# Performance work log

Hardware: AMD Instinct MI355X
Metric: run time of the kernel (lower is better)

Reference implementation:

```python
import jax, jax.numpy as jnp
import numpy as np
from jax import lax

D_MODEL = 1024
D_STATE = 128
D_CONV = 4
EXPAND = 2
HEADDIM = 64
D_INNER = EXPAND * D_MODEL          # 2048
NHEADS = D_INNER // HEADDIM         # 32
D_IN_PROJ = 2 * D_INNER + 2 * D_STATE + NHEADS  # 4384 (z, xBC, dt)
CONV_CH = D_INNER + 2 * D_STATE     # 2304
CHUNK = 128
EPS = 1e-5
BATCH, SEQ = 2, 2048


def silu(x):
    return x * jax.nn.sigmoid(x)


def rmsnorm(x, w):
    return x * lax.rsqrt(jnp.mean(x * x, axis=-1, keepdims=True) + EPS) * w


def segsum(a):
    # a: (b,h,c,q) -> (b,h,c,q,q); [i,j] = sum_{j<k<=i} a_k, -inf above diag
    q = a.shape[-1]
    cs = jnp.cumsum(a, axis=-1)
    seg = cs[..., :, None] - cs[..., None, :]
    mask = jnp.tril(jnp.ones((q, q), dtype=bool))
    return jnp.where(mask, seg, -jnp.inf)


def ssd(xh, dt, A, B, C):
    # xh: (b,l,h,p), dt: (b,l,h), A: (h,), B,C: (b,l,n). Chunked SSD scan.
    b, l, h, p = xh.shape
    n = B.shape[-1]
    c = l // CHUNK
    X = (xh * dt[..., None]).reshape(b, c, CHUNK, h, p)
    Adt = (A * dt).reshape(b, c, CHUNK, h).transpose(0, 3, 1, 2)  # (b,h,c,q)
    Bc = B.reshape(b, c, CHUNK, n)
    Cc = C.reshape(b, c, CHUNK, n)
    Acs = jnp.cumsum(Adt, axis=-1)
    L = jnp.exp(segsum(Adt))  # (b,h,c,q,q) causal decay within chunk
    Y_diag = jnp.einsum('bcln,bcsn,bhcls,bcshp->bclhp', Cc, Bc, L, X)
    decay_states = jnp.exp(Acs[..., -1:] - Acs)
    states = jnp.einsum('bcln,bhcl,bclhp->bchpn', Bc, decay_states, X)
    chunk_decay = jnp.exp(Acs[..., -1])  # (b,h,c)

    def step(s, inp):
        st, cd = inp
        return s * cd[:, :, None, None] + st, s

    init = jnp.zeros((b, h, p, n), dtype=xh.dtype)
    _, prev = lax.scan(step, init,
                       (states.transpose(1, 0, 2, 3, 4), chunk_decay.transpose(2, 0, 1)))
    # prev: (c,b,h,p,n) = state at start of each chunk
    Y_off = jnp.einsum('bcln,cbhpn,bhcl->bclhp', Cc, prev, jnp.exp(Acs))
    return (Y_diag + Y_off).reshape(b, l, h, p)


def mamba2(x, in_w, conv_w, conv_b, dt_bias, A_log, D, gnorm_w, out_w):
    b, l, _ = x.shape
    zxbcdt = x @ in_w.T  # (b,l,D_IN_PROJ)
    z = zxbcdt[..., :D_INNER]
    xBC = zxbcdt[..., D_INNER:D_INNER + CONV_CH]
    dt = jax.nn.softplus(zxbcdt[..., D_INNER + CONV_CH:] + dt_bias)  # (b,l,h)
    # causal depthwise conv1d
    xp = jnp.pad(xBC, ((0, 0), (D_CONV - 1, 0), (0, 0)))
    conv = sum(xp[:, k:k + l, :] * conv_w[:, k] for k in range(D_CONV)) + conv_b
    xBC = silu(conv)
    xs = xBC[..., :D_INNER]
    B = xBC[..., D_INNER:D_INNER + D_STATE]
    C = xBC[..., D_INNER + D_STATE:]
    A = -jnp.exp(A_log)
    xh = xs.reshape(b, l, NHEADS, HEADDIM)
    y = ssd(xh, dt, A, B, C) + xh * D[None, None, :, None]
    y = y.reshape(b, l, D_INNER)
    y = rmsnorm(y * silu(z), gnorm_w)  # RMSNormGated
    return y @ out_w.T


def setup_inputs() -> dict:
    key = jax.random.key(0)
    ks = jax.random.split(key, 24)
    d = {}
    d['x'] = jax.random.normal(ks[0], (BATCH, SEQ, D_MODEL), dtype=jnp.float32)
    d['norm_w'] = jnp.ones((D_MODEL,), jnp.float32)
    d['out_w_blk'] = jax.random.normal(ks[1], (D_MODEL, 2 * D_MODEL), jnp.float32) * 0.02
    d['out_b_blk'] = jnp.zeros((D_MODEL,), jnp.float32)
    for i, pfx in enumerate(['f_', 'b_']):
        o = 2 + i * 10
        d[pfx + 'in_w'] = jax.random.normal(ks[o], (D_IN_PROJ, D_MODEL), jnp.float32) * 0.02
        d[pfx + 'conv_w'] = jax.random.normal(ks[o + 1], (CONV_CH, D_CONV), jnp.float32) * 0.2
        d[pfx + 'conv_b'] = jnp.zeros((CONV_CH,), jnp.float32)
        d[pfx + 'dt_bias'] = jax.random.normal(ks[o + 2], (NHEADS,), jnp.float32) * 0.1
        d[pfx + 'A_log'] = jnp.log(jax.random.uniform(ks[o + 3], (NHEADS,), jnp.float32, 1.0, 16.0))
        d[pfx + 'D'] = jnp.ones((NHEADS,), jnp.float32)
        d[pfx + 'gnorm_w'] = jnp.ones((D_INNER,), jnp.float32)
        d[pfx + 'out_w'] = jax.random.normal(ks[o + 4], (D_MODEL, D_INNER), jnp.float32) * 0.02
    return d


def reference(x, norm_w, out_w_blk, out_b_blk,
              f_in_w, f_conv_w, f_conv_b, f_dt_bias, f_A_log, f_D, f_gnorm_w, f_out_w,
              b_in_w, b_conv_w, b_conv_b, b_dt_bias, b_A_log, b_D, b_gnorm_w, b_out_w):
    xn = rmsnorm(x, norm_w)
    y_fwd = mamba2(xn, f_in_w, f_conv_w, f_conv_b, f_dt_bias, f_A_log, f_D, f_gnorm_w, f_out_w)
    y_bwd = jnp.flip(
        mamba2(jnp.flip(xn, axis=1), b_in_w, b_conv_w, b_conv_b, b_dt_bias, b_A_log, b_D, b_gnorm_w, b_out_w),
        axis=1)
    out = jnp.concatenate([y_fwd, y_bwd], axis=-1) @ out_w_blk.T + out_b_blk
    return x + out
```

## Files before the change

### kernel.cpp

```cpp
#include <hip/hip_runtime.h>
#include <hip/hip_bf16.h>
#include <math.h>

#define BATCH 2
#define SEQL 2048
#define T 4096
#define DMODEL 1024
#define DINNER 2048
#define DSTATE 128
#define NH 32
#define HD 64
#define DPROJ2 4352
#define CONVCH 2304
#define NCH 16
#define CHUNK 128
#define EPS 1e-5f

#define N_INW ((size_t)DPROJ2 * DMODEL)
#define N_OUTW ((size_t)DMODEL * DINNER)
#define N_ST ((size_t)BATCH * NCH * NH * HD * DSTATE)
#define F2B_BLOCKS 10752
#define TW_BLOCKS 1024

typedef unsigned short u16;
typedef __bf16 bf16x8 __attribute__((ext_vector_type(8)));
typedef float f32x4 __attribute__((ext_vector_type(4)));

__device__ __forceinline__ u16 f2b(float f) {
    union { float f; unsigned u; } v; v.f = f;
    unsigned r = v.u + 0x7fffu + ((v.u >> 16) & 1u);
    return (u16)(r >> 16);
}
__device__ __forceinline__ float b2f(u16 b) {
    union { unsigned u; float f; } v; v.u = ((unsigned)b) << 16;
    return v.f;
}
__device__ __forceinline__ int flipseq(int r) {
    return (r & ~(SEQL - 1)) | ((SEQL - 1) - (r & (SEQL - 1)));
}
__device__ __forceinline__ void gload16(const u16* g, u16* l) {
    __builtin_amdgcn_global_load_lds(
        (const __attribute__((address_space(1))) void*)g,
        (__attribute__((address_space(3))) void*)l, 16, 0, 0);
}

#define FENCE asm volatile("" ::: "memory")

__device__ __forceinline__ float blockReduceSum(float v) {
    __shared__ float red_[4];
    for (int off = 32; off > 0; off >>= 1) v += __shfl_down(v, off);
    int lane = threadIdx.x & 63, wid = threadIdx.x >> 6;
    if (lane == 0) red_[wid] = v;
    __syncthreads();
    if (threadIdx.x == 0) {
        float s = 0.f;
        int nw = blockDim.x >> 6;
        for (int i = 0; i < nw; ++i) s += red_[i];
        red_[0] = s;
    }
    __syncthreads();
    return red_[0];
}

__global__ __launch_bounds__(256) void k_rmsdt(
    const float* __restrict__ x, const float* __restrict__ w,
    const float* __restrict__ inw_f, const float* __restrict__ inw_b,
    const float* __restrict__ dtb_f, const float* __restrict__ dtb_b,
    u16* __restrict__ outb, float* __restrict__ dt)
{
    __shared__ float xs[4][1024];
    int r0 = blockIdx.x * 4;
    int tid = threadIdx.x;
    int lane = tid & 63, wv = tid >> 6;
    int row = r0 + wv;
    const float* xr = x + (size_t)row * DMODEL;
    float4 v[4];
    float ss = 0.f;
    #pragma unroll
    for (int i = 0; i < 4; ++i) {
        v[i] = *(const float4*)(xr + (i * 64 + lane) * 4);
        ss += v[i].x * v[i].x + v[i].y * v[i].y + v[i].z * v[i].z + v[i].w * v[i].w;
    }
    #pragma unroll
    for (int off = 32; off > 0; off >>= 1) ss += __shfl_down(ss, off);
    ss = __shfl(ss, 0);
    float sc = rsqrtf(ss / DMODEL + EPS);
    #pragma unroll
    for (int i = 0; i < 4; ++i) {
        int c = (i * 64 + lane) * 4;
        float4 wv4 = *(const float4*)(w + c);
        ushort4 o;
        o.x = f2b(v[i].x * sc * wv4.x);
        o.y = f2b(v[i].y * sc * wv4.y);
        o.z = f2b(v[i].z * sc * wv4.z);
        o.w = f2b(v[i].w * sc * wv4.w);
        *(ushort4*)(outb + (size_t)row * DMODEL + c) = o;
        xs[wv][c + 0] = b2f(o.x); xs[wv][c + 1] = b2f(o.y);
        xs[wv][c + 2] = b2f(o.z); xs[wv][c + 3] = b2f(o.w);
    }
    __syncthreads();
    int h2 = tid >> 2, part = tid & 3;
    int dir = h2 >> 5, h = h2 & 31;
    const float* wd = (dir ? inw_b : inw_f) + (size_t)(DPROJ2 + h) * DMODEL;
    float a0 = 0.f, a1 = 0.f, a2 = 0.f, a3 = 0.f;
    for (int kk = 0; kk < 256; ++kk) {
        int k = part + (kk << 2);
        float wvv = wd[k];
        a0 += xs[0][k] * wvv; a1 += xs[1][k] * wvv;
        a2 += xs[2][k] * wvv; a3 += xs[3][k] * wvv;
    }
    #pragma unroll
    for (int off = 2; off > 0; off >>= 1) {
        a0 += __shfl_down(a0, off, 4); a1 += __shfl_down(a1, off, 4);
        a2 += __shfl_down(a2, off, 4); a3 += __shfl_down(a3, off, 4);
    }
    if (part == 0) {
        float bsh = dir ? dtb_b[h] : dtb_f[h];
        float* dtp = dt + (size_t)dir * T * NH;
        float vv[4] = {a0, a1, a2, a3};
        #pragma unroll
        for (int rr = 0; rr < 4; ++rr) {
            int rg = r0 + rr;
            if (dir) rg = flipseq(rg);
            float vvv = vv[rr] + bsh;
            dtp[(size_t)rg * NH + h] = (vvv > 20.f) ? vvv : log1pf(expf(vvv));
        }
    }
}

__global__ __launch_bounds__(256) void k_wprep(
    const float* __restrict__ f_in_w, const float* __restrict__ b_in_w,
    const float* __restrict__ out_w_blk,
    const float* __restrict__ f_out_w, const float* __restrict__ b_out_w,
    u16* __restrict__ d_inwb, u16* __restrict__ d_owbb, u16* __restrict__ d_fowT)
{
    __shared__ u16 t[64][65];
    int bid = blockIdx.x;
    if (bid < F2B_BLOCKS) {
        size_t i = ((size_t)bid * 256 + threadIdx.x) * 4;
        const float* s; u16* d; size_t off;
        if (i < 2 * N_INW) {
            int dir = i >= N_INW;
            off = i - (size_t)dir * N_INW;
            s = dir ? b_in_w : f_in_w; d = d_inwb + (size_t)dir * N_INW;
        } else {
            off = i - 2 * N_INW;
            if (off >= N_OUTW) return;
            s = out_w_blk; d = d_owbb;
        }
        float4 v = *(const float4*)(s + off);
        ushort4 o;
        o.x = f2b(v.x); o.y = f2b(v.y); o.z = f2b(v.z); o.w = f2b(v.w);
        *(ushort4*)(d + off) = o;
        return;
    }
    int b2 = bid - F2B_BLOCKS;
    int dir = b2 >> 9;
    int rem = b2 & 511;
    int c0 = (rem & 31) * 64, e0 = (rem >> 5) * 64;
    const float* src = dir ? b_out_w : f_out_w;
    u16* d = d_fowT + (size_t)dir * N_OUTW;
    for (int i = threadIdx.x; i < 64 * 16; i += 256) {
        int el = i >> 4, c4 = (i & 15) * 4;
        float4 v = *(const float4*)(src + (size_t)(e0 + el) * DINNER + c0 + c4);
        t[c4 + 0][el] = f2b(v.x); t[c4 + 1][el] = f2b(v.y);
        t[c4 + 2][el] = f2b(v.z); t[c4 + 3][el] = f2b(v.w);
    }
    __syncthreads();
    for (int i = threadIdx.x; i < 64 * 16; i += 256) {
        int cl = i >> 4, e4 = (i & 15) * 4;
        ushort4 o;
        o.x = t[cl][e4]; o.y = t[cl][e4 + 1]; o.z = t[cl][e4 + 2]; o.w = t[cl][e4 + 3];
        *(ushort4*)(d + (size_t)(c0 + cl) * DMODEL + e0 + e4) = o;
    }
}

__global__ __launch_bounds__(512, 2) void k_mm_in8(
    const u16* __restrict__ A, const u16* __restrict__ W0,
    u16* __restrict__ zb0, u16* __restrict__ xbcraw0)
{
    __shared__ u16 lds_[8 * 8192];
    int dir = blockIdx.z;
    const u16* W = W0 + (size_t)dir * N_INW;

    int f = blockIdx.x + (blockIdx.y << 4);
    int xcd = f & 7;
    int jj = f >> 3;
    int m0 = (jj >> 1) * 256;
    int n0 = ((xcd << 1) | (jj & 1)) * 256;

    u16* Cout; int ldcc, nbase;
    if (n0 < DINNER) {
        Cout = zb0 + (size_t)dir * T * DINNER;
        ldcc = DINNER;
        nbase = n0;
    } else {
        Cout = xbcraw0 + (size_t)dir * T * CONVCH;
        ldcc = CONVCH;
        nbase = n0 - DINNER;
    }

    int tid = threadIdx.x;
    int lane = tid & 63;
    int w = tid >> 6;
    int wm = w >> 2;
    int wn = w & 3;
    int l15 = lane & 15;
    int gsw0 = (((lane >> 4) ^ (lane & 7)) << 3);
    int gsw1 = (((4 + (lane >> 4)) ^ (lane & 7)) << 3);

    const u16* pA[2][2];
    const u16* pB[2][2];
    int swz = ((lane & 7) ^ (lane >> 3)) << 3;
    #pragma unroll
    for (int h = 0; h < 2; ++h)
        #pragma unroll
        for (int c = 0; c < 2; ++c) {
            int rl = (w * 2 + c) * 8 + (lane >> 3);
            int grow = m0 + h * 128 + rl;
            if (dir) grow = flipseq(grow);
            pA[h][c] = A + (size_t)grow * DMODEL + swz;
            pB[h][c] = W + (size_t)(n0 + h * 128 + rl) * DMODEL + swz;
        }
    int dst0 = (w * 2 + 0) * 512 + lane * 8;
    int dst1 = (w * 2 + 1) * 512 + lane * 8;

#define STAGE_A(t_, h_) do { \
        gload16(pA[h_][0] + (t_) * 64, lds_ + (((t_) & 1) * 4 + (h_)) * 8192 + dst0); \
        gload16(pA[h_][1] + (t_) * 64, lds_ + (((t_) & 1) * 4 + (h_)) * 8192 + dst1); \
    } while (0)
#define STAGE_B(t_, h_) do { \
        gload16(pB[h_][0] + (t_) * 64, lds_ + (((t_) & 1) * 4 + 2 + (h_)) * 8192 + dst0); \
        gload16(pB[h_][1] + (t_) * 64, lds_ + (((t_) & 1) * 4 + 2 + (h_)) * 8192 + dst1); \
    } while (0)

    f32x4 acc[8][4] = {};
    bf16x8 bfv[4][2];

    STAGE_A(0, 0); STAGE_A(0, 1); STAGE_B(0, 0); STAGE_B(0, 1);
    FENCE;
    STAGE_B(1, 0); STAGE_B(1, 1);
    asm volatile("s_waitcnt vmcnt(4)" ::: "memory");
    __builtin_amdgcn_s_barrier();
    FENCE;

    for (int kt = 0; kt < 16; ++kt) {
        int d = kt & 1;
        const u16* Ab = lds_ + (d * 4 + wm) * 8192;
        const u16* Bb = lds_ + (d * 4 + 2 + (wn >> 1)) * 8192;
        int nrow0 = (wn & 1) * 64;
        #pragma unroll
        for (int q = 0; q < 4; ++q) {
            if (q == 0) {
                #pragma unroll
                for (int j = 0; j < 4; ++j) {
                    const u16* bp = Bb + (nrow0 + j * 16 + l15) * 64;
                    bfv[j][0] = *(const bf16x8*)(bp + gsw0);
                    bfv[j][1] = *(const bf16x8*)(bp + gsw1);
                }
            }
            const u16* ap0 = Ab + ((q * 2 + 0) * 16 + l15) * 64;
            const u16* ap1 = Ab + ((q * 2 + 1) * 16 + l15) * 64;
            bf16x8 a0k0 = *(const bf16x8*)(ap0 + gsw0);
            bf16x8 a0k1 = *(const bf16x8*)(ap0 + gsw1);
            bf16x8 a1k0 = *(const bf16x8*)(ap1 + gsw0);
            bf16x8 a1k1 = *(const bf16x8*)(ap1 + gsw1);
            if (q == 0)      { if (kt < 15) STAGE_A(kt + 1, 0); }
            else if (q == 1) { if (kt < 15) STAGE_A(kt + 1, 1); }
            else if (q == 2) { if (kt < 14) STAGE_B(kt + 2, 0); }
            else             { if (kt < 14) STAGE_B(kt + 2, 1); }
            FENCE;
            __builtin_amdgcn_s_barrier();
            asm volatile("s_waitcnt lgkmcnt(0)" ::: "memory");
            __builtin_amdgcn_s_setprio(1);
            #pragma unroll
            for (int j = 0; j < 4; ++j) {
                acc[q * 2 + 0][j] = __builtin_amdgcn_mfma_f32_16x16x32_bf16(a0k0, bfv[j][0], acc[q * 2 + 0][j], 0, 0, 0);
                acc[q * 2 + 0][j] = __builtin_amdgcn_mfma_f32_16x16x32_bf16(a0k1, bfv[j][1], acc[q * 2 + 0][j], 0, 0, 0);
                acc[q * 2 + 1][j] = __builtin_amdgcn_mfma_f32_16x16x32_bf16(a1k0, bfv[j][0], acc[q * 2 + 1][j], 0, 0, 0);
                acc[q * 2 + 1][j] = __builtin_amdgcn_mfma_f32_16x16x32_bf16(a1k1, bfv[j][1], acc[q * 2 + 1][j], 0, 0, 0);
            }
            __builtin_amdgcn_s_setprio(0);
            if (q == 3) {
                if (kt < 14)       asm volatile("s_waitcnt vmcnt(4)" ::: "memory");
                else if (kt == 14) asm volatile("s_waitcnt vmcnt(0)" ::: "memory");
            }
            FENCE;
            __builtin_amdgcn_s_barrier();
            FENCE;
        }
    }
#undef STAGE_A
#undef STAGE_B

    int rb = m0 + wm * 128 + ((lane >> 4) << 2);
    int cb = nbase + wn * 64 + l15;
    #pragma unroll
    for (int i = 0; i < 8; ++i)
        #pragma unroll
        for (int j = 0; j < 4; ++j)
            #pragma unroll
            for (int r = 0; r < 4; ++r)
                Cout[(size_t)(rb + i * 16 + r) * ldcc + cb + j * 16] = f2b(acc[i][j][r]);
}

__global__ __launch_bounds__(256, 4) void k_mm_in(
    const u16* __restrict__ A, const u16* __restrict__ W0,
    u16* __restrict__ zb0, u16* __restrict__ xbcraw0, int ny0)
{
    const int K = DMODEL;
    int dir = blockIdx.z;
    const u16* W = W0 + (size_t)dir * N_INW;
    int m0 = blockIdx.x * 128, n0 = (blockIdx.y + ny0) * 128;

    u16* Cout;
    int ldcc, nbase;
    if (n0 < DINNER) {
        Cout = zb0 + (size_t)dir * T * DINNER;
        ldcc = DINNER;
        nbase = n0;
    } else {
        Cout = xbcraw0 + (size_t)dir * T * CONVCH;
        ldcc = CONVCH;
        nbase = n0 - DINNER;
    }

    __shared__ u16 As[2 * 128 * 32];
    __shared__ u16 Bs[2 * 128 * 32];
    int tid = threadIdx.x;
    int lane = tid & 63;
    int wrow = ((tid >> 6) & 1) * 64, wcol = (tid >> 7) * 64;

    int srow = tid >> 2, skof = (tid & 3) * 8;
    int ar1 = m0 + srow, ar2 = ar1 + 64;
    if (dir) { ar1 = flipseq(ar1); ar2 = flipseq(ar2); }
    const u16* ga1 = A + (size_t)ar1 * K + skof;
    const u16* ga2 = A + (size_t)ar2 * K + skof;
    const u16* gb1 = W + (size_t)(n0 + srow) * K + skof;
    const u16* gb2 = gb1 + (size_t)64 * K;
    u16* la1 = As + tid * 8;
    u16* la2 = As + 2048 + tid * 8;
    u16* lb1 = Bs + tid * 8;
    u16* lb2 = Bs + 2048 + tid * 8;

    int aoff[4], boff[4];
    #pragma unroll
    for (int i = 0; i < 4; ++i) {
        aoff[i] = (wrow + i * 16 + (lane & 15)) * 32 + ((lane >> 4) * 8);
        boff[i] = (wcol + i * 16 + (lane & 15)) * 32 + ((lane >> 4) * 8);
    }

    f32x4 acc[4][4] = {};
    for (int kt = 0; kt < K; kt += 64) {
        gload16(ga1, la1);        gload16(ga2, la2);
        gload16(ga1 + 32, la1 + 4096); gload16(ga2 + 32, la2 + 4096);
        gload16(gb1, lb1);        gload16(gb2, lb2);
        gload16(gb1 + 32, lb1 + 4096); gload16(gb2 + 32, lb2 + 4096);
        ga1 += 64; ga2 += 64; gb1 += 64; gb2 += 64;
        __syncthreads();
        #pragma unroll
        for (int ks = 0; ks < 2; ++ks) {
            bf16x8 af[4], bfv[4];
            #pragma unroll
            for (int i = 0; i < 4; ++i) af[i] = *(const bf16x8*)(As + ks * 4096 + aoff[i]);
            #pragma unroll
            for (int j = 0; j < 4; ++j) bfv[j] = *(const bf16x8*)(Bs + ks * 4096 + boff[j]);
            #pragma unroll
            for (int i = 0; i < 4; ++i)
                #pragma unroll
                for (int j = 0; j < 4; ++j)
                    acc[i][j] = __builtin_amdgcn_mfma_f32_16x16x32_bf16(af[i], bfv[j], acc[i][j], 0, 0, 0);
        }
        __syncthreads();
    }

    int rbase = m0 + wrow + ((lane >> 4) << 2);
    int cbase = nbase + wcol + (lane & 15);
    #pragma unroll
    for (int i = 0; i < 4; ++i)
        #pragma unroll
        for (int j = 0; j < 4; ++j)
            #pragma unroll
            for (int r = 0; r < 4; ++r)
                Cout[(size_t)(rbase + i * 16 + r) * ldcc + cbase + j * 16] = f2b(acc[i][j][r]);
}

__global__ __launch_bounds__(256) void k_mm64(
    const u16* __restrict__ A0, const u16* __restrict__ W0,
    u16* __restrict__ Cb)
{
    int dir = blockIdx.z;
    const u16* A = A0 + dir * DMODEL;
    const u16* W = W0 + (size_t)dir * N_OUTW;

    __shared__ u16 As[2 * 128 * 32];
    __shared__ u16 Bs[2 * 64 * 32];
    int tid = threadIdx.x;
    int lane = tid & 63;
    int w = tid >> 6;
    int m0 = blockIdx.y * 128, n0 = blockIdx.x * 64;
    int wrow = (w & 1) * 64, wcol = (w >> 1) * 32;

    int srow = tid >> 2, skof = (tid & 3) * 8;
    const u16* ga1 = A + (size_t)(m0 + srow) * 2048 + skof;
    const u16* ga2 = A + (size_t)(m0 + 64 + srow) * 2048 + skof;
    const u16* gb  = W + (size_t)(n0 + srow) * DMODEL + skof;
    u16* la1 = As + tid * 8;
    u16* la2 = As + 2048 + tid * 8;
    u16* lb  = Bs + tid * 8;

    int aoff[4], boff[2];
    #pragma unroll
    for (int i = 0; i < 4; ++i)
        aoff[i] = (wrow + i * 16 + (lane & 15)) * 32 + ((lane >> 4) * 8);
    #pragma unroll
    for (int j = 0; j < 2; ++j)
        boff[j] = (wcol + j * 16 + (lane & 15)) * 32 + ((lane >> 4) * 8);

    f32x4 acc[4][2] = {};
    for (int kt = 0; kt < DMODEL; kt += 64) {
        gload16(ga1, la1); gload16(ga1 + 32, la1 + 4096);
        gload16(ga2, la2); gload16(ga2 + 32, la2 + 4096);
        gload16(gb, lb);   gload16(gb + 32, lb + 2048);
        ga1 += 64; ga2 += 64; gb += 64;
        __syncthreads();
        #pragma unroll
        for (int ks = 0; ks < 2; ++ks) {
            bf16x8 af[4], bfv[2];
            #pragma unroll
            for (int i = 0; i < 4; ++i) af[i] = *(const bf16x8*)(As + ks * 4096 + aoff[i]);
            #pragma unroll
            for (int j = 0; j < 2; ++j) bfv[j] = *(const bf16x8*)(Bs + ks * 2048 + boff[j]);
            #pragma unroll
            for (int i = 0; i < 4; ++i)
                #pragma unroll
                for (int j = 0; j < 2; ++j)
                    acc[i][j] = __builtin_amdgcn_mfma_f32_16x16x32_bf16(af[i], bfv[j], acc[i][j], 0, 0, 0);
        }
        __syncthreads();
    }

    int rbase = m0 + wrow + ((lane >> 4) << 2);
    int cbase = n0 + wcol + (lane & 15);
    #pragma unroll
    for (int i = 0; i < 4; ++i)
        #pragma unroll
        for (int j = 0; j < 2; ++j)
            #pragma unroll
            for (int r = 0; r < 4; ++r)
                Cb[(size_t)(rbase + i * 16 + r) * 4096 + dir * 2048 + cbase + j * 16] = f2b(acc[i][j][r]);
}

__global__ __launch_bounds__(256) void k_mm_fin(
    const u16* __restrict__ A1, const u16* __restrict__ A2,
    const u16* __restrict__ W,
    float* __restrict__ out, const float* __restrict__ bias,
    const float* __restrict__ resid)
{
    __shared__ u16 As[4 * 128 * 32];
    __shared__ u16 Bs[2 * 2 * 64 * 32];
    int tid = threadIdx.x;
    int lane = tid & 63;
    int w = tid >> 6;
    int m0 = blockIdx.y * 128, n0 = blockIdx.x * 64;
    int wrow = (w & 1) * 64, wcol = (w >> 1) * 32;

    int srow = tid >> 2, skof = (tid & 3) * 8;
    const u16* ga1  = A1 + (size_t)(m0 + srow) * DINNER + skof;
    const u16* ga1b = A1 + (size_t)(m0 + 64 + srow) * DINNER + skof;
    const u16* ga2  = A2 + (size_t)flipseq(m0 + srow) * DINNER + skof;
    const u16* ga2b = A2 + (size_t)flipseq(m0 + 64 + srow) * DINNER + skof;
    const u16* gb1 = W + (size_t)(n0 + srow) * 4096 + skof;
    const u16* gb2 = gb1 + 2048;
    u16* la1  = As + tid * 8;
    u16* la1b = As + 2048 + tid * 8;
    u16* la2  = As + 8192 + tid * 8;
    u16* la2b = As + 8192 + 2048 + tid * 8;
    u16* lb1 = Bs + tid * 8;
    u16* lb2 = Bs + 4096 + tid * 8;

    int aoff[4], boff[2];
    #pragma unroll
    for (int i = 0; i < 4; ++i)
        aoff[i] = (wrow + i * 16 + (lane & 15)) * 32 + ((lane >> 4) * 8);
    #pragma unroll
    for (int j = 0; j < 2; ++j)
        boff[j] = (wcol + j * 16 + (lane & 15)) * 32 + ((lane >> 4) * 8);

    f32x4 acc[4][2] = {};
    for (int kt = 0; kt < DINNER; kt += 64) {
        gload16(ga1, la1);    gload16(ga1 + 32, la1 + 4096);
        gload16(ga1b, la1b);  gload16(ga1b + 32, la1b + 4096);
        gload16(ga2, la2);    gload16(ga2 + 32, la2 + 4096);
        gload16(ga2b, la2b);  gload16(ga2b + 32, la2b + 4096);
        gload16(gb1, lb1);    gload16(gb1 + 32, lb1 + 2048);
        gload16(gb2, lb2);    gload16(gb2 + 32, lb2 + 2048);
        ga1 += 64; ga1b += 64; ga2 += 64; ga2b += 64; gb1 += 64; gb2 += 64;
        __syncthreads();
        #pragma unroll
        for (int h = 0; h < 2; ++h) {
            #pragma unroll
            for (int ks = 0; ks < 2; ++ks) {
                bf16x8 af[4], bfv[2];
                #pragma unroll
                for (int i = 0; i < 4; ++i)
                    af[i] = *(const bf16x8*)(As + h * 8192 + ks * 4096 + aoff[i]);
                #pragma unroll
                for (int j = 0; j < 2; ++j)
                    bfv[j] = *(const bf16x8*)(Bs + h * 4096 + ks * 2048 + boff[j]);
                #pragma unroll
                for (int i = 0; i < 4; ++i)
                    #pragma unroll
                    for (int j = 0; j < 2; ++j)
                        acc[i][j] = __builtin_amdgcn_mfma_f32_16x16x32_bf16(af[i], bfv[j], acc[i][j], 0, 0, 0);
            }
        }
        __syncthreads();
    }

    int rbase = m0 + wrow + ((lane >> 4) << 2);
    int cbase = n0 + wcol + (lane & 15);
    #pragma unroll
    for (int i = 0; i < 4; ++i)
        #pragma unroll
        for (int j = 0; j < 2; ++j)
            #pragma unroll
            for (int r = 0; r < 4; ++r) {
                int row = rbase + i * 16 + r, col = cbase + j * 16;
                out[(size_t)row * DMODEL + col] =
                    acc[i][j][r] + bias[col] + resid[(size_t)row * DMODEL + col];
            }
}

__global__ void k_conv(const u16* __restrict__ xraw0,
                       const float* __restrict__ cw_f, const float* __restrict__ cw_b,
                       const float* __restrict__ cb_f, const float* __restrict__ cb_b,
                       const float* __restrict__ dt0,
                       u16* __restrict__ xbcb0, u16* __restrict__ xdtb0)
{
    int dir = blockIdx.z;
    const u16* xraw = xraw0 + (size_t)dir * T * CONVCH;
    const float* cw = dir ? cw_b : cw_f;
    const float* cb = dir ? cb_b : cb_f;
    const float* dt = dt0 + (size_t)dir * T * NH;
    u16* xbcb = xbcb0 + (size_t)dir * T * CONVCH;
    u16* xdtb = xdtb0 + (size_t)dir * T * DINNER;

    int idx = blockIdx.x * blockDim.x + threadIdx.x;
    if (idx >= (T / 4) * (CONVCH / 8)) return;
    int r4 = idx / (CONVCH / 8);
    int c8 = (idx - r4 * (CONVCH / 8)) * 8;
    int r0 = r4 * 4;
    int t0 = r0 & (SEQL - 1);

    float4 cwv[8];
    #pragma unroll
    for (int j = 0; j < 8; ++j) cwv[j] = *(const float4*)(cw + (size_t)(c8 + j) * 4);
    float acc[4][8];
    {
        float4 c0 = *(const float4*)(cb + c8);
        float4 c1 = *(const float4*)(cb + c8 + 4);
        #pragma unroll
        for (int i = 0; i < 4; ++i) {
            acc[i][0] = c0.x; acc[i][1] = c0.y; acc[i][2] = c0.z; acc[i][3] = c0.w;
            acc[i][4] = c1.x; acc[i][5] = c1.y; acc[i][6] = c1.z; acc[i][7] = c1.w;
        }
    }
    #pragma unroll
    for (int s = 0; s < 7; ++s) {
        int tt = t0 - 3 + s;
        if (tt < 0) continue;
        const u16* src = xraw + (size_t)(r0 - 3 + s) * CONVCH + c8;
        ushort4 v0 = *(const ushort4*)src;
        ushort4 v1 = *(const ushort4*)(src + 4);
        float xv[8] = {b2f(v0.x), b2f(v0.y), b2f(v0.z), b2f(v0.w),
                       b2f(v1.x), b2f(v1.y), b2f(v1.z), b2f(v1.w)};
        #pragma unroll
        for (int i = 0; i < 4; ++i) {
            if (i <= s && i >= s - 3) {
                const int j = s - i;
                #pragma unroll
                for (int ch = 0; ch < 8; ++ch) {
                    float wv = (j == 0) ? cwv[ch].x : (j == 1) ? cwv[ch].y
                             : (j == 2) ? cwv[ch].z : cwv[ch].w;
                    acc[i][ch] += xv[ch] * wv;
                }
            }
        }
    }
    #pragma unroll
    for (int i = 0; i < 4; ++i) {
        int r = r0 + i;
        float sgl[8];
        #pragma unroll
        for (int ch = 0; ch < 8; ++ch) sgl[ch] = acc[i][ch] / (1.f + __expf(-acc[i][ch]));
        ushort4 o0, o1;
        o0.x = f2b(sgl[0]); o0.y = f2b(sgl[1]); o0.z = f2b(sgl[2]); o0.w = f2b(sgl[3]);
        o1.x = f2b(sgl[4]); o1.y = f2b(sgl[5]); o1.z = f2b(sgl[6]); o1.w = f2b(sgl[7]);
        *(ushort4*)(xbcb + (size_t)r * CONVCH + c8) = o0;
        *(ushort4*)(xbcb + (size_t)r * CONVCH + c8 + 4) = o1;
        if (c8 < DINNER) {
            float dv = dt[(size_t)r * NH + (c8 >> 6)];
            ushort4 d0, d1;
            d0.x = f2b(sgl[0] * dv); d0.y = f2b(sgl[1] * dv);
            d0.z = f2b(sgl[2] * dv); d0.w = f2b(sgl[3] * dv);
            d1.x = f2b(sgl[4] * dv); d1.y = f2b(sgl[5] * dv);
            d1.z = f2b(sgl[6] * dv); d1.w = f2b(sgl[7] * dv);
            *(ushort4*)(xdtb + (size_t)r * DINNER + c8) = d0;
            *(ushort4*)(xdtb + (size_t)r * DINNER + c8 + 4) = d1;
        }
    }
}

#define LDW 136
__global__ __launch_bounds__(256) void k_states(
    const u16* __restrict__ xbcb0, const u16* __restrict__ xdtb0,
    const float* __restrict__ dt0,
    const float* __restrict__ Alog_f, const float* __restrict__ Alog_b,
    float* __restrict__ acs0, float* __restrict__ cd0, u16* __restrict__ st0)
{
    int dir = blockIdx.z;
    const u16* xbcb = xbcb0 + (size_t)dir * T * CONVCH;
    const u16* xdtb = xdtb0 + (size_t)dir * T * DINNER;
    const float* dt = dt0 + (size_t)dir * T * NH;
    const float* A_log = dir ? Alog_b : Alog_f;
    float* acs = acs0 + (size_t)dir * BATCH * NH * NCH * CHUNK;
    float* cd = cd0 + (size_t)dir * BATCH * NH * NCH;
    u16* st = st0 + (size_t)dir * N_ST;

    __shared__ u16 Bt[128 * LDW];
    __shared__ u16 Xt[64 * LDW];
    __shared__ float cs[128];
    __shared__ float dec_s[128];
    int tid = threadIdx.x;
    int lane = tid & 63;
    int w = tid >> 6;
    int h = blockIdx.x & 31;
    int bc = blockIdx.x >> 5;
    int c = bc & 15, b = bc >> 4;
    int row0 = b * SEQL + c * CHUNK;

    if (tid < 128) {
        float Ah = -expf(A_log[h]);
        cs[tid] = Ah * dt[(size_t)(row0 + tid) * NH + h];
    }
    for (int i = tid; i < 128 * 16; i += 256) {
        int l = i >> 4, pg = (i & 15) * 4;
        ushort4 v = *(const ushort4*)(xdtb + (size_t)(row0 + l) * DINNER + h * HD + pg);
        Xt[(pg + 0) * LDW + l] = v.x; Xt[(pg + 1) * LDW + l] = v.y;
        Xt[(pg + 2) * LDW + l] = v.z; Xt[(pg + 3) * LDW + l] = v.w;
    }
    __syncthreads();
    for (int off = 1; off < 128; off <<= 1) {
        float tval = 0.f;
        if (tid < 128 && tid >= off) tval = cs[tid - off];
        __syncthreads();
        if (tid < 128) cs[tid] += tval;
        __syncthreads();
    }
    size_t abase = ((size_t)(b * NH + h) * NCH + c) << 7;
    if (tid < 128) acs[abase + tid] = cs[tid];
    float a_last = cs[127];
    if (tid == 127) cd[(b * NH + h) * NCH + c] = expf(a_last);
    if (tid < 128) dec_s[tid] = __expf(a_last - cs[tid]);
    __syncthreads();
    for (int i = tid; i < 128 * 32; i += 256) {
        int l = i >> 5, ng = (i & 31) * 4;
        ushort4 v = *(const ushort4*)(xbcb + (size_t)(row0 + l) * CONVCH + DINNER + ng);
        float d = dec_s[l];
        Bt[(ng + 0) * LDW + l] = f2b(b2f(v.x) * d);
        Bt[(ng + 1) * LDW + l] = f2b(b2f(v.y) * d);
        Bt[(ng + 2) * LDW + l] = f2b(b2f(v.z) * d);
        Bt[(ng + 3) * LDW + l] = f2b(b2f(v.w) * d);
    }
    __syncthreads();
    f32x4 tacc[8] = {};
    for (int kk = 0; kk < 4; ++kk) {
        bf16x8 afs = *(const bf16x8*)(Xt + (w * 16 + (lane & 15)) * LDW
                                      + kk * 32 + (lane >> 4) * 8);
        #pragma unroll
        for (int j = 0; j < 8; ++j) {
// ... 100 lines not shown
    for (int i = 0; i < 4; ++i)
        #pragma unroll
        for (int j = 0; j < 4; ++j) {
            int s = wcol + j * 16 + (lane & 15);
            #pragma unroll
            for (int r = 0; r < 4; ++r) {
                int l = wrow + i * 16 + (lane >> 4) * 4 + r;
                float v = (s <= l) ? sacc[i][j][r] * __expf(acs_s[l] - acs_s[s]) : 0.f;
                S0[l * LDW + s] = f2b(v);
            }
        }
    __syncthreads();
    f32x4 yacc[2][4] = {};
    for (int kk = 0; kk < 4; ++kk) {
        bf16x8 af[2], bfr[4];
        #pragma unroll
        for (int i = 0; i < 2; ++i)
            af[i] = *(const bf16x8*)(S0 + (w * 32 + i * 16 + (lane & 15)) * LDW
                                     + kk * 32 + (lane >> 4) * 8);
        #pragma unroll
        for (int j = 0; j < 4; ++j)
            bfr[j] = *(const bf16x8*)(Xt + (j * 16 + (lane & 15)) * LDW
                                      + kk * 32 + (lane >> 4) * 8);
        #pragma unroll
        for (int i = 0; i < 2; ++i)
            #pragma unroll
            for (int j = 0; j < 4; ++j)
                yacc[i][j] = __builtin_amdgcn_mfma_f32_16x16x32_bf16(af[i], bfr[j], yacc[i][j], 0, 0, 0);
    }
    __syncthreads();
    size_t sb = (size_t)blockIdx.x * (HD * DSTATE);
    for (int i = tid; i < 64 * 16; i += 256) {
        int p = i >> 4, m8 = (i & 15) * 8;
        *(uint4*)(S0 + p * LDW + m8) = *(const uint4*)(prev + sb + (size_t)p * DSTATE + m8);
    }
    __syncthreads();
    f32x4 oacc[2][4] = {};
    for (int kk = 0; kk < 4; ++kk) {
        bf16x8 af[2], bfr[4];
        #pragma unroll
        for (int i = 0; i < 2; ++i)
            af[i] = *(const bf16x8*)(cbase + (size_t)(w * 32 + i * 16 + (lane & 15)) * CONVCH
                                     + kk * 32 + (lane >> 4) * 8);
        #pragma unroll
        for (int j = 0; j < 4; ++j)
            bfr[j] = *(const bf16x8*)(S0 + (j * 16 + (lane & 15)) * LDW
                                      + kk * 32 + (lane >> 4) * 8);
        #pragma unroll
        for (int i = 0; i < 2; ++i)
            #pragma unroll
            for (int j = 0; j < 4; ++j)
                oacc[i][j] = __builtin_amdgcn_mfma_f32_16x16x32_bf16(af[i], bfr[j], oacc[i][j], 0, 0, 0);
    }
    float Dh = Dp[h];
    #pragma unroll
    for (int i = 0; i < 2; ++i)
        #pragma unroll
        for (int j = 0; j < 4; ++j)
            #pragma unroll
            for (int r = 0; r < 4; ++r) {
                int l = w * 32 + i * 16 + (lane >> 4) * 4 + r;
                int p = j * 16 + (lane & 15);
                float val = yacc[i][j][r] + __expf(acs_s[l]) * oacc[i][j][r]
                          + b2f(xbcb[(size_t)(row0 + l) * CONVCH + h * HD + p]) * Dh;
                y[(size_t)(row0 + l) * DINNER + h * HD + p] = f2b(val);
            }
}

__global__ __launch_bounds__(256) void k_gate(
    const u16* __restrict__ y0, const u16* __restrict__ zb0,
    const float* __restrict__ gw_f, const float* __restrict__ gw_b,
    u16* __restrict__ out0)
{
    int dir = blockIdx.z;
    const u16* y = y0 + (size_t)dir * T * DINNER;
    const u16* zb = zb0 + (size_t)dir * T * DINNER;
    const float* gw = dir ? gw_b : gw_f;
    u16* out = out0 + (size_t)dir * T * DINNER;

    int r = blockIdx.x;
    int tid = threadIdx.x;
    float tv[8];
    float ss = 0.f;
    #pragma unroll
    for (int it = 0; it < 2; ++it) {
        int i = (it * 256 + tid) * 4;
        ushort4 yv = *(const ushort4*)(y + (size_t)r * DINNER + i);
        ushort4 zv = *(const ushort4*)(zb + (size_t)r * DINNER + i);
        float z0 = b2f(zv.x), z1 = b2f(zv.y), z2 = b2f(zv.z), z3 = b2f(zv.w);
        float t0 = b2f(yv.x) * (z0 / (1.f + __expf(-z0)));
        float t1 = b2f(yv.y) * (z1 / (1.f + __expf(-z1)));
        float t2 = b2f(yv.z) * (z2 / (1.f + __expf(-z2)));
        float t3 = b2f(yv.w) * (z3 / (1.f + __expf(-z3)));
        tv[it * 4 + 0] = t0; tv[it * 4 + 1] = t1; tv[it * 4 + 2] = t2; tv[it * 4 + 3] = t3;
        ss += t0 * t0 + t1 * t1 + t2 * t2 + t3 * t3;
    }
    float tot = blockReduceSum(ss);
    float sc = rsqrtf(tot / DINNER + EPS);
    #pragma unroll
    for (int it = 0; it < 2; ++it) {
        int i = (it * 256 + tid) * 4;
        ushort4 o;
        o.x = f2b(tv[it * 4 + 0] * sc * gw[i]);
        o.y = f2b(tv[it * 4 + 1] * sc * gw[i + 1]);
        o.z = f2b(tv[it * 4 + 2] * sc * gw[i + 2]);
        o.w = f2b(tv[it * 4 + 3] * sc * gw[i + 3]);
        *(ushort4*)(out + (size_t)r * DINNER + i) = o;
    }
}

extern "C" void kernel_launch(void* const* d_in, const int* in_sizes, int n_in,
                              void* d_out, int out_size, void* d_ws, size_t ws_size,
                              hipStream_t stream)
{
    const float* x         = (const float*)d_in[0];
    const float* norm_w    = (const float*)d_in[1];
    const float* out_w_blk = (const float*)d_in[2];
    const float* out_b_blk = (const float*)d_in[3];
    const float* f_in_w    = (const float*)d_in[4];
    const float* f_conv_w  = (const float*)d_in[5];
    const float* f_conv_b  = (const float*)d_in[6];
    const float* f_dt_bias = (const float*)d_in[7];
    const float* f_A_log   = (const float*)d_in[8];
    const float* f_D       = (const float*)d_in[9];
    const float* f_gnorm_w = (const float*)d_in[10];
    const float* f_out_w   = (const float*)d_in[11];
    const float* b_in_w    = (const float*)d_in[12];
    const float* b_conv_w  = (const float*)d_in[13];
    const float* b_conv_b  = (const float*)d_in[14];
    const float* b_dt_bias = (const float*)d_in[15];
    const float* b_A_log   = (const float*)d_in[16];
    const float* b_D       = (const float*)d_in[17];
    const float* b_gnorm_w = (const float*)d_in[18];
    const float* b_out_w   = (const float*)d_in[19];
    float* out = (float*)d_out;

    char* ws = (char*)d_ws;
    u16*  xnb    = (u16*)ws;   ws += (size_t)T * DMODEL * 2;
    u16*  zb     = (u16*)ws;   ws += (size_t)2 * T * DINNER * 2;
    u16*  xbcraw = (u16*)ws;   ws += (size_t)2 * T * CONVCH * 2;
    u16*  xbcb   = (u16*)ws;   ws += (size_t)2 * T * CONVCH * 2;
    u16*  xdtb   = (u16*)ws;   ws += (size_t)2 * T * DINNER * 2;
    float* dtb   = (float*)ws; ws += (size_t)2 * T * NH * 4;
    float* acs   = (float*)ws; ws += (size_t)2 * BATCH * NH * NCH * CHUNK * 4;
    float* cd    = (float*)ws; ws += (size_t)2 * BATCH * NH * NCH * 4;
    u16*  stb    = (u16*)ws;   ws += (size_t)2 * N_ST * 2;
    u16*  inwb   = (u16*)ws;   ws += (size_t)2 * N_INW * 2;
    u16*  fowT2  = (u16*)ws;   ws += (size_t)2 * N_OUTW * 2;
    u16*  owbb   = (u16*)ws;   ws += (size_t)N_OUTW * 2;
    u16*  yb16  = xbcraw;
    u16*  ybb   = xdtb;
    u16*  Mcomb = xbcb;

    k_rmsdt<<<T / 4, 256, 0, stream>>>(x, norm_w, f_in_w, b_in_w,
                                       f_dt_bias, b_dt_bias, xnb, dtb);
    k_wprep<<<F2B_BLOCKS + TW_BLOCKS, 256, 0, stream>>>(
        f_in_w, b_in_w, out_w_blk, f_out_w, b_out_w, inwb, owbb, fowT2);

    {
        dim3 g(T / 256, 16, 2);
        k_mm_in8<<<g, 512, 0, stream>>>(xnb, inwb, zb, xbcraw);
    }
    {
        dim3 g(T / 128, 2, 2);
        k_mm_in<<<g, 256, 0, stream>>>(xnb, inwb, zb, xbcraw, 32);
    }
    {
        dim3 g(((T / 4) * (CONVCH / 8) + 255) / 256, 1, 2);
        k_conv<<<g, 256, 0, stream>>>(xbcraw, f_conv_w, b_conv_w, f_conv_b, b_conv_b,
                                      dtb, xbcb, xdtb);
    }
    {
        dim3 g(BATCH * NCH * NH, 1, 2);
        k_states<<<g, 256, 0, stream>>>(xbcb, xdtb, dtb, f_A_log, b_A_log, acs, cd, stb);
    }
    k_scan<<<(2 * BATCH * NH * HD * DSTATE) / 256, 256, 0, stream>>>(stb, cd);
    {
        dim3 g(BATCH * NCH * NH, 1, 2);
        k_chunk<<<g, 256, 0, stream>>>(xbcb, xdtb, acs, stb, f_D, b_D, yb16);
    }
    {
        dim3 g(T, 1, 2);
        k_gate<<<g, 256, 0, stream>>>(yb16, zb, f_gnorm_w, b_gnorm_w, ybb);
    }
    {
        dim3 g(DINNER / 64, DMODEL / 128, 2);
        k_mm64<<<g, 256, 0, stream>>>(owbb, fowT2, Mcomb);
    }
    {
        dim3 g(DMODEL / 64, T / 128, 1);
        k_mm_fin<<<g, 256, 0, stream>>>(ybb, ybb + (size_t)T * DINNER, Mcomb,
                                        out, out_b_blk, x);
    }
}
```

Before: 507.3 us.

## Merge prep kernels, XCD-remap mm64, and rewrite final GEMM as pipelined 8-wave kernel

Merges the RMSnorm/dt kernel and the weight-prep kernel into one launch, which removes a launch and lets the two independent jobs overlap. It remaps k_mm64 blocks to a 1D grid with an XCD-aware tile assignment. It also replaces the final output GEMM with a 512-thread, 128x128-tile kernel that uses double-buffered async global-to-LDS loads, a swizzled LDS layout, explicit waitcnt/barrier scheduling and setprio around the MFMAs. The new GEMM depends on careful hand synchronisation and uses more LDS per block.

```diff
diff --git a/kernel.cpp b/kernel.cpp
--- a/kernel.cpp
+++ b/kernel.cpp
@@ -62,82 +62,81 @@
     return red_[0];
 }
 
-__global__ __launch_bounds__(256) void k_rmsdt(
+__global__ __launch_bounds__(256) void k_prep(
     const float* __restrict__ x, const float* __restrict__ w,
-    const float* __restrict__ inw_f, const float* __restrict__ inw_b,
+    const float* __restrict__ f_in_w, const float* __restrict__ b_in_w,
     const float* __restrict__ dtb_f, const float* __restrict__ dtb_b,
-    u16* __restrict__ outb, float* __restrict__ dt)
-{
-    __shared__ float xs[4][1024];
-    int r0 = blockIdx.x * 4;
-    int tid = threadIdx.x;
-    int lane = tid & 63, wv = tid >> 6;
-    int row = r0 + wv;
-    const float* xr = x + (size_t)row * DMODEL;
-    float4 v[4];
-    float ss = 0.f;
-    #pragma unroll
-    for (int i = 0; i < 4; ++i) {
-        v[i] = *(const float4*)(xr + (i * 64 + lane) * 4);
-        ss += v[i].x * v[i].x + v[i].y * v[i].y + v[i].z * v[i].z + v[i].w * v[i].w;
-    }
-    #pragma unroll
-    for (int off = 32; off > 0; off >>= 1) ss += __shfl_down(ss, off);
-    ss = __shfl(ss, 0);
-    float sc = rsqrtf(ss / DMODEL + EPS);
-    #pragma unroll
-    for (int i = 0; i < 4; ++i) {
-        int c = (i * 64 + lane) * 4;
-        float4 wv4 = *(const float4*)(w + c);
-        ushort4 o;
-        o.x = f2b(v[i].x * sc * wv4.x);
-        o.y = f2b(v[i].y * sc * wv4.y);
-        o.z = f2b(v[i].z * sc * wv4.z);
-        o.w = f2b(v[i].w * sc * wv4.w);
-        *(ushort4*)(outb + (size_t)row * DMODEL + c) = o;
-        xs[wv][c + 0] = b2f(o.x); xs[wv][c + 1] = b2f(o.y);
-        xs[wv][c + 2] = b2f(o.z); xs[wv][c + 3] = b2f(o.w);
-    }
-    __syncthreads();
-    int h2 = tid >> 2, part = tid & 3;
-    int dir = h2 >> 5, h = h2 & 31;
-    const float* wd = (dir ? inw_b : inw_f) + (size_t)(DPROJ2 + h) * DMODEL;
-    float a0 = 0.f, a1 = 0.f, a2 = 0.f, a3 = 0.f;
-    for (int kk = 0; kk < 256; ++kk) {
-        int k = part + (kk << 2);
-        float wvv = wd[k];
-        a0 += xs[0][k] * wvv; a1 += xs[1][k] * wvv;
-        a2 += xs[2][k] * wvv; a3 += xs[3][k] * wvv;
-    }
-    #pragma unroll
-    for (int off = 2; off > 0; off >>= 1) {
-        a0 += __shfl_down(a0, off, 4); a1 += __shfl_down(a1, off, 4);
-        a2 += __shfl_down(a2, off, 4); a3 += __shfl_down(a3, off, 4);
-    }
-    if (part == 0) {
-        float bsh = dir ? dtb_b[h] : dtb_f[h];
-        float* dtp = dt + (size_t)dir * T * NH;
-        float vv[4] = {a0, a1, a2, a3};
-        #pragma unroll
-        for (int rr = 0; rr < 4; ++rr) {
-            int rg = r0 + rr;
-            if (dir) rg = flipseq(rg);
-            float vvv = vv[rr] + bsh;
-            dtp[(size_t)rg * NH + h] = (vvv > 20.f) ? vvv : log1pf(expf(vvv));
-        }
-    }
-}
-
-__global__ __launch_bounds__(256) void k_wprep(
-    const float* __restrict__ f_in_w, const float* __restrict__ b_in_w,
+    u16* __restrict__ outb, float* __restrict__ dt,
     const float* __restrict__ out_w_blk,
     const float* __restrict__ f_out_w, const float* __restrict__ b_out_w,
     u16* __restrict__ d_inwb, u16* __restrict__ d_owbb, u16* __restrict__ d_fowT)
 {
+    __shared__ float xs[4][1024];
     __shared__ u16 t[64][65];
-    int bid = blockIdx.x;
+    int bid0 = blockIdx.x;
+    int tid = threadIdx.x;
+    if (bid0 < 1024) {
+        int r0 = bid0 * 4;
+        int lane = tid & 63, wv = tid >> 6;
+        int row = r0 + wv;
+        const float* xr = x + (size_t)row * DMODEL;
+        float4 v[4];
+        float ss = 0.f;
+        #pragma unroll
+        for (int i = 0; i < 4; ++i) {
+            v[i] = *(const float4*)(xr + (i * 64 + lane) * 4);
+            ss += v[i].x * v[i].x + v[i].y * v[i].y + v[i].z * v[i].z + v[i].w * v[i].w;
+        }
+        #pragma unroll
+        for (int off = 32; off > 0; off >>= 1) ss += __shfl_down(ss, off);
+        ss = __shfl(ss, 0);
+        float sc = rsqrtf(ss / DMODEL + EPS);
+        #pragma unroll
+        for (int i = 0; i < 4; ++i) {
+            int c = (i * 64 + lane) * 4;
+            float4 wv4 = *(const float4*)(w + c);
+            ushort4 o;
+            o.x = f2b(v[i].x * sc * wv4.x);
+            o.y = f2b(v[i].y * sc * wv4.y);
+            o.z = f2b(v[i].z * sc * wv4.z);
+            o.w = f2b(v[i].w * sc * wv4.w);
+            *(ushort4*)(outb + (size_t)row * DMODEL + c) = o;
+            xs[wv][c + 0] = b2f(o.x); xs[wv][c + 1] = b2f(o.y);
+            xs[wv][c + 2] = b2f(o.z); xs[wv][c + 3] = b2f(o.w);
+        }
+        __syncthreads();
+        int h2 = tid >> 2, part = tid & 3;
+        int dir = h2 >> 5, h = h2 & 31;
+        const float* wd = (dir ? b_in_w : f_in_w) + (size_t)(DPROJ2 + h) * DMODEL;
+        float a0 = 0.f, a1 = 0.f, a2 = 0.f, a3 = 0.f;
+        for (int kk = 0; kk < 256; ++kk) {
+            int k = part + (kk << 2);
+            float wvv = wd[k];
+            a0 += xs[0][k] * wvv; a1 += xs[1][k] * wvv;
+            a2 += xs[2][k] * wvv; a3 += xs[3][k] * wvv;
+        }
+        #pragma unroll
+        for (int off = 2; off > 0; off >>= 1) {
+            a0 += __shfl_down(a0, off, 4); a1 += __shfl_down(a1, off, 4);
+            a2 += __shfl_down(a2, off, 4); a3 += __shfl_down(a3, off, 4);
+        }
+        if (part == 0) {
+            float bsh = dir ? dtb_b[h] : dtb_f[h];
+            float* dtp = dt + (size_t)dir * T * NH;
+            float vv[4] = {a0, a1, a2, a3};
+            #pragma unroll
+            for (int rr = 0; rr < 4; ++rr) {
+                int rg = r0 + rr;
+                if (dir) rg = flipseq(rg);
+                float vvv = vv[rr] + bsh;
+                dtp[(size_t)rg * NH + h] = (vvv > 20.f) ? vvv : log1pf(expf(vvv));
+            }
+        }
+        return;
+    }
+    int bid = bid0 - 1024;
     if (bid < F2B_BLOCKS) {
-        size_t i = ((size_t)bid * 256 + threadIdx.x) * 4;
+        size_t i = ((size_t)bid * 256 + tid) * 4;
         const float* s; u16* d; size_t off;
         if (i < 2 * N_INW) {
             int dir = i >= N_INW;
@@ -160,14 +159,14 @@
     int c0 = (rem & 31) * 64, e0 = (rem >> 5) * 64;
     const float* src = dir ? b_out_w : f_out_w;
     u16* d = d_fowT + (size_t)dir * N_OUTW;
-    for (int i = threadIdx.x; i < 64 * 16; i += 256) {
+    for (int i = tid; i < 64 * 16; i += 256) {
         int el = i >> 4, c4 = (i & 15) * 4;
         float4 v = *(const float4*)(src + (size_t)(e0 + el) * DINNER + c0 + c4);
         t[c4 + 0][el] = f2b(v.x); t[c4 + 1][el] = f2b(v.y);
         t[c4 + 2][el] = f2b(v.z); t[c4 + 3][el] = f2b(v.w);
     }
     __syncthreads();
-    for (int i = threadIdx.x; i < 64 * 16; i += 256) {
+    for (int i = tid; i < 64 * 16; i += 256) {
         int cl = i >> 4, e4 = (i & 15) * 4;
         ushort4 o;
         o.x = t[cl][e4]; o.y = t[cl][e4 + 1]; o.z = t[cl][e4 + 2]; o.w = t[cl][e4 + 3];
@@ -389,7 +388,12 @@
     const u16* __restrict__ A0, const u16* __restrict__ W0,
     u16* __restrict__ Cb)
 {
-    int dir = blockIdx.z;
+    int bid = blockIdx.x;
+    int xcd = bid & 7;
+    int j9 = bid >> 3;
+    int dir = j9 >> 5;
+    int m0 = xcd * 128;
+    int n0 = (j9 & 31) * 64;
     const u16* A = A0 + dir * DMODEL;
     const u16* W = W0 + (size_t)dir * N_OUTW;
 
@@ -398,7 +402,6 @@
     int tid = threadIdx.x;
     int lane = tid & 63;
     int w = tid >> 6;
-    int m0 = blockIdx.y * 128, n0 = blockIdx.x * 64;
     int wrow = (w & 1) * 64, wcol = (w >> 1) * 32;
 
     int srow = tid >> 2, skof = (tid & 3) * 8;
@@ -451,82 +454,120 @@
                 Cb[(size_t)(rbase + i * 16 + r) * 4096 + dir * 2048 + cbase + j * 16] = f2b(acc[i][j][r]);
 }
 
-__global__ __launch_bounds__(256) void k_mm_fin(
+__global__ __launch_bounds__(512, 2) void k_mm_fin8(
     const u16* __restrict__ A1, const u16* __restrict__ A2,
     const u16* __restrict__ W,
     float* __restrict__ out, const float* __restrict__ bias,
     const float* __restrict__ resid)
 {
-    __shared__ u16 As[4 * 128 * 32];
-    __shared__ u16 Bs[2 * 2 * 64 * 32];
+    __shared__ u16 lds_[8 * 8192];
+    int bid = blockIdx.x;
+    int xcd = bid & 7;
+    int j9 = bid >> 3;
+    int m0 = (xcd * 4 + (j9 & 3)) * 128;
+    int n0 = (j9 >> 2) * 128;
     int tid = threadIdx.x;
     int lane = tid & 63;
     int w = tid >> 6;
-    int m0 = blockIdx.y * 128, n0 = blockIdx.x * 64;
-    int wrow = (w & 1) * 64, wcol = (w >> 1) * 32;
-
-    int srow = tid >> 2, skof = (tid & 3) * 8;
-    const u16* ga1  = A1 + (size_t)(m0 + srow) * DINNER + skof;
-    const u16* ga1b = A1 + (size_t)(m0 + 64 + srow) * DINNER + skof;
-    const u16* ga2  = A2 + (size_t)flipseq(m0 + srow) * DINNER + skof;
-    const u16* ga2b = A2 + (size_t)flipseq(m0 + 64 + srow) * DINNER + skof;
-    const u16* gb1 = W + (size_t)(n0 + srow) * 4096 + skof;
-    const u16* gb2 = gb1 + 2048;
-    u16* la1  = As + tid * 8;
-    u16* la1b = As + 2048 + tid * 8;
-    u16* la2  = As + 8192 + tid * 8;
-    u16* la2b = As + 8192 + 2048 + tid * 8;
-    u16* lb1 = Bs + tid * 8;
-    u16* lb2 = Bs + 4096 + tid * 8;
-
-    int aoff[4], boff[2];
+    int wm = w >> 2;
+    int wn = w & 3;
+    int l15 = lane & 15;
+    int gsw0 = (((lane >> 4) ^ (lane & 7)) << 3);
+    int gsw1 = (((4 + (lane >> 4)) ^ (lane & 7)) << 3);
+
+    const u16* p[4][2];
+    int swz = ((lane & 7) ^ (lane >> 3)) << 3;
+    #pragma unroll
+    for (int c = 0; c < 2; ++c) {
+        int rl = (w * 2 + c) * 8 + (lane >> 3);
+        p[0][c] = A1 + (size_t)(m0 + rl) * DINNER + swz;
+        p[1][c] = A2 + (size_t)flipseq(m0 + rl) * DINNER + swz;
+        p[2][c] = W + (size_t)(n0 + rl) * 4096 + swz;
+        p[3][c] = p[2][c] + 2048;
+    }
+    int dst0 = (w * 2 + 0) * 512 + lane * 8;
+    int dst1 = (w * 2 + 1) * 512 + lane * 8;
+
+#define STG(t_, s_) do { \
+        gload16(p[s_][0] + (t_) * 64, lds_ + (((t_) & 1) * 4 + (s_)) * 8192 + dst0); \
+        gload16(p[s_][1] + (t_) * 64, lds_ + (((t_) & 1) * 4 + (s_)) * 8192 + dst1); \
+    } while (0)
+
+    f32x4 acc[4][2] = {};
+    bf16x8 bf1[2][2], bf2[2][2];
+
+    STG(0, 0); STG(0, 1); STG(0, 2); STG(0, 3);
+    FENCE;
+    STG(1, 2); STG(1, 3);
+    asm volatile("s_waitcnt vmcnt(4)" ::: "memory");
+    __builtin_amdgcn_s_barrier();
+    FENCE;
+
+    for (int kt = 0; kt < 32; ++kt) {
+        int d = kt & 1;
+        const u16* A1b = lds_ + (d * 4 + 0) * 8192;
+        const u16* A2b = lds_ + (d * 4 + 1) * 8192;
+        const u16* B1b = lds_ + (d * 4 + 2) * 8192;
+        const u16* B2b = lds_ + (d * 4 + 3) * 8192;
+        #pragma unroll
+        for (int ph = 0; ph < 2; ++ph) {
+            if (ph == 0) {
+                #pragma unroll
+                for (int j = 0; j < 2; ++j) {
+                    const u16* bp1 = B1b + (wn * 32 + j * 16 + l15) * 64;
+                    const u16* bp2 = B2b + (wn * 32 + j * 16 + l15) * 64;
+                    bf1[j][0] = *(const bf16x8*)(bp1 + gsw0);
+                    bf1[j][1] = *(const bf16x8*)(bp1 + gsw1);
+                    bf2[j][0] = *(const bf16x8*)(bp2 + gsw0);
+                    bf2[j][1] = *(const bf16x8*)(bp2 + gsw1);
+                }
+            }
+            bf16x8 a1[2][2], a2[2][2];
+            #pragma unroll
+            for (int i = 0; i < 2; ++i) {
+                int ro = (wm * 64 + (ph * 2 + i) * 16 + l15) * 64;
+                a1[i][0] = *(const bf16x8*)(A1b + ro + gsw0);
+                a1[i][1] = *(const bf16x8*)(A1b + ro + gsw1);
+                a2[i][0] = *(const bf16x8*)(A2b + ro + gsw0);
+                a2[i][1] = *(const bf16x8*)(A2b + ro + gsw1);
+            }
+            if (ph == 0) { if (kt < 31) { STG(kt + 1, 0); STG(kt + 1, 1); } }
+            else         { if (kt < 30) { STG(kt + 2, 2); STG(kt + 2, 3); } }
+            FENCE;
+            __builtin_amdgcn_s_barrier();
+            asm volatile("s_waitcnt lgkmcnt(0)" ::: "memory");
+            __builtin_amdgcn_s_setprio(1);
+            #pragma unroll
+            for (int i = 0; i < 2; ++i)
+                #pragma unroll
+                for (int j = 0; j < 2; ++j) {
+                    int q = ph * 2 + i;
+                    acc[q][j] = __builtin_amdgcn_mfma_f32_16x16x32_bf16(a1[i][0], bf1[j][0], acc[q][j], 0, 0, 0);
+                    acc[q][j] = __builtin_amdgcn_mfma_f32_16x16x32_bf16(a1[i][1], bf1[j][1], acc[q][j], 0, 0, 0);
+                    acc[q][j] = __builtin_amdgcn_mfma_f32_16x16x32_bf16(a2[i][0], bf2[j][0], acc[q][j], 0, 0, 0);
+                    acc[q][j] = __builtin_amdgcn_mfma_f32_16x16x32_bf16(a2[i][1], bf2[j][1], acc[q][j], 0, 0, 0);
+                }
+            __builtin_amdgcn_s_setprio(0);
+            if (ph == 1) {
+                if (kt < 30)       asm volatile("s_waitcnt vmcnt(4)" ::: "memory");
+                else if (kt == 30) asm volatile("s_waitcnt vmcnt(0)" ::: "memory");
+            }
+            FENCE;
+            __builtin_amdgcn_s_barrier();
+            FENCE;
+        }
+    }
+#undef STG
+
+    int rb = m0 + wm * 64 + ((lane >> 4) << 2);
+    int cb = n0 + wn * 32 + l15;
     #pragma unroll
     for (int i = 0; i < 4; ++i)
-        aoff[i] = (wrow + i * 16 + (lane & 15)) * 32 + ((lane >> 4) * 8);
-    #pragma unroll
-    for (int j = 0; j < 2; ++j)
-        boff[j] = (wcol + j * 16 + (lane & 15)) * 32 + ((lane >> 4) * 8);
-
-    f32x4 acc[4][2] = {};
-    for (int kt = 0; kt < DINNER; kt += 64) {
-        gload16(ga1, la1);    gload16(ga1 + 32, la1 + 4096);
-        gload16(ga1b, la1b);  gload16(ga1b + 32, la1b + 4096);
-        gload16(ga2, la2);    gload16(ga2 + 32, la2 + 4096);
-        gload16(ga2b, la2b);  gload16(ga2b + 32, la2b + 4096);
-        gload16(gb1, lb1);    gload16(gb1 + 32, lb1 + 2048);
-        gload16(gb2, lb2);    gload16(gb2 + 32, lb2 + 2048);
-        ga1 += 64; ga1b += 64; ga2 += 64; ga2b += 64; gb1 += 64; gb2 += 64;
-        __syncthreads();
-        #pragma unroll
-        for (int h = 0; h < 2; ++h) {
-            #pragma unroll
-            for (int ks = 0; ks < 2; ++ks) {
-                bf16x8 af[4], bfv[2];
-                #pragma unroll
-                for (int i = 0; i < 4; ++i)
-                    af[i] = *(const bf16x8*)(As + h * 8192 + ks * 4096 + aoff[i]);
-                #pragma unroll
-                for (int j = 0; j < 2; ++j)
-                    bfv[j] = *(const bf16x8*)(Bs + h * 4096 + ks * 2048 + boff[j]);
-                #pragma unroll
-                for (int i = 0; i < 4; ++i)
-                    #pragma unroll
-                    for (int j = 0; j < 2; ++j)
-                        acc[i][j] = __builtin_amdgcn_mfma_f32_16x16x32_bf16(af[i], bfv[j], acc[i][j], 0, 0, 0);
-            }
-        }
-        __syncthreads();
-    }
-
-    int rbase = m0 + wrow + ((lane >> 4) << 2);
-    int cbase = n0 + wcol + (lane & 15);
-    #pragma unroll
-    for (int i = 0; i < 4; ++i)
         #pragma unroll
         for (int j = 0; j < 2; ++j)
             #pragma unroll
             for (int r = 0; r < 4; ++r) {
-                int row = rbase + i * 16 + r, col = cbase + j * 16;
+                int row = rb + i * 16 + r, col = cb + j * 16;
                 out[(size_t)row * DMODEL + col] =
                     acc[i][j][r] + bias[col] + resid[(size_t)row * DMODEL + col];
             }
@@ -933,10 +974,9 @@
     u16*  ybb   = xdtb;
     u16*  Mcomb = xbcb;
 
-    k_rmsdt<<<T / 4, 256, 0, stream>>>(x, norm_w, f_in_w, b_in_w,
-                                       f_dt_bias, b_dt_bias, xnb, dtb);
-    k_wprep<<<F2B_BLOCKS + TW_BLOCKS, 256, 0, stream>>>(
-        f_in_w, b_in_w, out_w_blk, f_out_w, b_out_w, inwb, owbb, fowT2);
+    k_prep<<<1024 + F2B_BLOCKS + TW_BLOCKS, 256, 0, stream>>>(
+        x, norm_w, f_in_w, b_in_w, f_dt_bias, b_dt_bias, xnb, dtb,
+        out_w_blk, f_out_w, b_out_w, inwb, owbb, fowT2);
 
     {
         dim3 g(T / 256, 16, 2);
@@ -964,13 +1004,7 @@
         dim3 g(T, 1, 2);
         k_gate<<<g, 256, 0, stream>>>(yb16, zb, f_gnorm_w, b_gnorm_w, ybb);
     }
-    {
-        dim3 g(DINNER / 64, DMODEL / 128, 2);
-        k_mm64<<<g, 256, 0, stream>>>(owbb, fowT2, Mcomb);
-    }
-    {
-        dim3 g(DMODEL / 64, T / 128, 1);
-        k_mm_fin<<<g, 256, 0, stream>>>(ybb, ybb + (size_t)T * DINNER, Mcomb,
-                                        out, out_b_blk, x);
-    }
-}
+    k_mm64<<<512, 256, 0, stream>>>(owbb, fowT2, Mcomb);
+    k_mm_fin8<<<256, 512, 0, stream>>>(ybb, ybb + (size_t)T * DINNER, Mcomb,
+                                       out, out_b_blk, x);
+}
```

Measured after the change: 487.2 us. 1.04x faster.
